# Kernel optimization log

Hardware: AMD Instinct MI355X
Metric: run time of the kernel (lower is better)

## Reference

```python
import jax, jax.numpy as jnp
import numpy as np

W_SEG = 2048   # segment_length w
R = 4          # dilation r
H = 16         # num_attention_heads


def setup_inputs() -> dict:
    key = jax.random.key(0)
    k0, k1, k2 = jax.random.split(key, 3)
    B, S, Hid = 2, 8192, 1024
    X = jax.random.normal(k0, (B, S, Hid), dtype=jnp.float32)
    Wq = jax.random.normal(k1, (Hid, Hid), dtype=jnp.float32) * 0.02
    bq = jnp.zeros((Hid,), jnp.float32)
    Wkv = jax.random.normal(k2, (Hid, 2 * Hid), dtype=jnp.float32) * 0.02
    bkv = jnp.zeros((2 * Hid,), jnp.float32)
    return {"X": X, "Wq": Wq, "bq": bq, "Wkv": Wkv, "bkv": bkv}


def reference(X, Wq, bq, Wkv, bkv):
    B, S, Hid = X.shape
    D = Hid // H                      # head dim
    num_points = W_SEG // R           # tokens kept per segment
    num_seg = S // W_SEG
    scale = 1.0 / np.sqrt(D).astype(np.float32)

    q = (X @ Wq + bq).reshape(B, S, H, D)
    kv = (X @ Wkv + bkv).reshape(B, S, 2, H, D)
    k, v = kv[:, :, 0], kv[:, :, 1]

    # dilated base indices: segment offset + r-strided points -> [num_seg*num_points]
    base = (jnp.arange(num_seg)[:, None] * W_SEG
            + jnp.arange(num_points)[None, :] * R).reshape(-1)
    shift = jnp.arange(H) % R                       # per-head shift
    idx = base[None, :] + shift[:, None]            # [H, T']
    Tq = idx.shape[1]
    idxT = idx.T                                    # [T', H]
    head_ix = jnp.arange(H)[None, :]                # [1, H] -> broadcasts with idxT

    # per-head dilated gather: sparse[b, t, h, d] = full[b, idx[h, t], h, d]
    sq = q[:, idxT, head_ix, :]                     # [B, T', H, D]
    sk = k[:, idxT, head_ix, :]
    sv = v[:, idxT, head_ix, :]

    sq = sq.reshape(B, num_seg, num_points, H, D)
    sk = sk.reshape(B, num_seg, num_points, H, D)
    sv = sv.reshape(B, num_seg, num_points, H, D)

    # per-segment (non-causal) attention, same math as flash_attn_kvpacked_func
    scores = jnp.einsum('bsqhd,bskhd->bshqk', sq, sk) * scale
    probs = jax.nn.softmax(scores, axis=-1)
    ctx = jnp.einsum('bshqk,bskhd->bsqhd', probs, sv)
    ctx = ctx.reshape(B, Tq, H, D)

    # scatter back into zeros at the gathered positions (unique per head)
    out = jnp.zeros((B, S, H, D), ctx.dtype).at[:, idxT, head_ix, :].set(ctx)
    return out.reshape(B, S, Hid)
```

## Files before the change

kernel.cpp:

```cpp
#include <hip/hip_runtime.h>

typedef unsigned short u16;
typedef unsigned int   u32;
typedef __bf16 bf16x8 __attribute__((ext_vector_type(8)));
typedef float  f32x4  __attribute__((ext_vector_type(4)));
typedef short  s16x4  __attribute__((ext_vector_type(4)));

#define QSCALE 0.125f

__device__ __forceinline__ u16 f2bf(float f) {
  union { float f; u32 u; } a; a.f = f;
  u32 u = a.u;
  u = (u + 0x7FFFu + ((u >> 16) & 1u)) >> 16;
  return (u16)u;
}

__device__ __forceinline__ void async16(const void* g, void* l) {
  __builtin_amdgcn_global_load_lds(
      (const __attribute__((address_space(1))) void*)g,
      (__attribute__((address_space(3))) void*)l, 16, 0, 0);
}

__global__ __launch_bounds__(256) void pack_w(const float* __restrict__ Wq,
                                              const float* __restrict__ Wkv,
                                              u16* __restrict__ Wp,
                                              const float* __restrict__ bq,
                                              const float* __restrict__ bkv,
                                              float* __restrict__ bp) {
  __shared__ float tile[32][65];
  int bx = blockIdx.x;
  if (bx >= 1536) {
    int idx = (bx - 1536) * 256 + threadIdx.x;
    int r = idx / 768, n = idx % 768;
    int t = n >> 8, hh = (n >> 6) & 3, d = n & 63;
    int h = hh * 4 + r;
    float v = (t == 0) ? bq[h * 64 + d] * QSCALE
            : (t == 1) ? bkv[h * 64 + d]
                       : bkv[1024 + h * 64 + d];
    bp[idx] = v;
    return;
  }
  int ks = bx & 31; int rem = bx >> 5;
  int hh = rem & 3; rem >>= 2;
  int t  = rem % 3; int r = rem / 3;
  int h  = hh * 4 + r;
  const float* src; int rs, cb;
  if (t == 0)      { src = Wq;  rs = 1024; cb = h * 64; }
  else if (t == 1) { src = Wkv; rs = 2048; cb = h * 64; }
  else             { src = Wkv; rs = 2048; cb = 1024 + h * 64; }
  int tid = threadIdx.x;
  {
    int kk = tid >> 3, dd = (tid & 7) << 3;
    const float* s0 = src + (size_t)(ks * 32 + kk) * rs + cb + dd;
    float4 a = *(const float4*)s0;
    float4 c = *(const float4*)(s0 + 4);
    tile[kk][dd + 0] = a.x; tile[kk][dd + 1] = a.y;
    tile[kk][dd + 2] = a.z; tile[kk][dd + 3] = a.w;
    tile[kk][dd + 4] = c.x; tile[kk][dd + 5] = c.y;
    tile[kk][dd + 6] = c.z; tile[kk][dd + 7] = c.w;
  }
  __syncthreads();
  {
    int d = tid >> 2, kc = tid & 3;
    float sc = (t == 0) ? QSCALE : 1.0f;
    u32 w[4];
#pragma unroll
    for (int j = 0; j < 4; ++j) {
      u16 lo = f2bf(tile[kc * 8 + 2 * j][d] * sc);
      u16 hi = f2bf(tile[kc * 8 + 2 * j + 1][d] * sc);
      w[j] = (u32)lo | ((u32)hi << 16);
    }
    int n = t * 256 + hh * 64 + d;
    int Nt = n >> 7, nt = (n >> 4) & 7, nn = n & 15;
    size_t off = (size_t)r * 786432 + (size_t)Nt * 131072 +
                 (size_t)ks * 4096 + nt * 512 + kc * 128 + nn * 8;
    uint4 o; o.x = w[0]; o.y = w[1]; o.z = w[2]; o.w = w[3];
    *(uint4*)(Wp + off) = o;
  }
}

__global__ __launch_bounds__(256, 3) void gemm1(const float* __restrict__ X,
                                                const u16* __restrict__ Wp,
                                                const float* __restrict__ bp,
                                                u16* __restrict__ Qd,
                                                u16* __restrict__ Kd,
                                                u16* __restrict__ Vd) {
  __shared__ u16 ldsAB[8192];
  u16* ldsA = ldsAB;
  u16* ldsB = ldsAB + 4096;
  int bx = blockIdx.x;
  int xcd = bx & 7;
  int idx = bx >> 3;
  int r = xcd >> 1;
  int Mtile = (xcd & 1) * 16 + (idx / 6);
  int Ntile = idx % 6;
  int tid = threadIdx.x, w = tid >> 6, lane = tid & 63;
  int wr = w >> 1, wc = w & 1;
  int l15 = lane & 15, l4 = lane >> 4;

  int rl = tid >> 1, tq = tid & 1;
  int srow = (Mtile >> 2) * 2048 + ((Mtile & 3) * 128 + rl) * 4 + r;
  const float* Xthr = X + (size_t)srow * 1024 + tq * 4;
  int abase = ((rl >> 4) * 64 + (rl & 15)) * 8 + tq * 4;

  const u16* Bsrc = Wp + (size_t)r * 786432 + (size_t)Ntile * 131072 +
                    w * 1024 + lane * 8;

  float4 ar[4];
#pragma unroll
  for (int it = 0; it < 4; ++it) ar[it] = *(const float4*)(Xthr + it * 8);

  f32x4 acc[4][4] = {};
  for (int ks = 0; ks < 32; ++ks) {
    __syncthreads();
#pragma unroll
    for (int it = 0; it < 4; ++it) {
      u32 x0 = __float_as_uint(ar[it].x) + 0x8000u;
      u32 x1 = __float_as_uint(ar[it].y) + 0x8000u;
      u32 x2 = __float_as_uint(ar[it].z) + 0x8000u;
      u32 x3 = __float_as_uint(ar[it].w) + 0x8000u;
      u32 lo = __builtin_amdgcn_perm(x1, x0, 0x07060302u);
      u32 hi = __builtin_amdgcn_perm(x3, x2, 0x07060302u);
      uint2 d2; d2.x = lo; d2.y = hi;
      *(uint2*)&ldsA[abase + it * 128] = d2;
    }
    const u16* b = Bsrc + ks * 4096;
    async16(b,       &ldsB[w * 1024]);
    async16(b + 512, &ldsB[w * 1024 + 512]);
    if (ks < 31) {
      const float* xn = Xthr + (ks + 1) * 32;
#pragma unroll
      for (int it = 0; it < 4; ++it) ar[it] = *(const float4*)(xn + it * 8);
    }
    __syncthreads();
    bf16x8 af[4], bf[4];
#pragma unroll
    for (int i = 0; i < 4; ++i)
      af[i] = *(const bf16x8*)&ldsA[((wr * 4 + i) * 64 + lane) * 8];
#pragma unroll
    for (int j = 0; j < 4; ++j)
      bf[j] = *(const bf16x8*)&ldsB[((wc * 4 + j) * 64 + lane) * 8];
#pragma unroll
    for (int i = 0; i < 4; ++i)
#pragma unroll
      for (int j = 0; j < 4; ++j)
        acc[i][j] = __builtin_amdgcn_mfma_f32_16x16x32_bf16(af[i], bf[j],
                                                            acc[i][j], 0, 0, 0);
  }

  int nb = Ntile * 128 + wc * 64;
  int t = nb >> 8, hh = (nb >> 6) & 3;
  int h = hh * 4 + r;
  u16* T = (t == 0) ? Qd : ((t == 1) ? Kd : Vd);
  float biasv[4];
#pragma unroll
  for (int j = 0; j < 4; ++j) biasv[j] = bp[r * 768 + nb + j * 16 + l15];

  u16* eb = ldsAB + w * 1152;
  int rrow = lane >> 2, seg = lane & 3;
#pragma unroll
  for (int i = 0; i < 4; ++i) {
    __syncthreads();
#pragma unroll
    for (int j = 0; j < 4; ++j)
#pragma unroll
      for (int reg = 0; reg < 4; ++reg)
        eb[(l4 * 4 + reg) * 72 + j * 16 + l15] = f2bf(acc[i][j][reg] + biasv[j]);
    __syncthreads();
    uint4 d0 = *(const uint4*)&eb[rrow * 72 + seg * 16];
    uint4 d1 = *(const uint4*)&eb[rrow * 72 + seg * 16 + 8];
    int m = Mtile * 128 + wr * 64 + i * 16 + rrow;
    int bseg = m >> 9, p = m & 511;
    size_t off = ((size_t)(bseg * 16 + h) * 512 + p) * 64 + seg * 16;
    *(uint4*)(T + off) = d0;
    *(uint4*)(T + off + 8) = d1;
  }
}

__global__ __launch_bounds__(512, 4) void attn(const u16* __restrict__ Qd,
                                               const u16* __restrict__ Kd,
                                               const u16* __restrict__ Vd,
                                               float* __restrict__ out) {
  __shared__ u16 ldsK[128 * 72];
  __shared__ u16 ldsV[64 * 136];
  int bx = blockIdx.x;
  int unit = bx & 127, qq = bx >> 7;
  int b = unit >> 6, seg = (unit >> 4) & 3, h = unit & 15;
  int tid = threadIdx.x, w = tid >> 6, lane = tid & 63;
  int l15 = lane & 15, l4 = lane >> 4;
  const u16* Qu = Qd + (size_t)unit * 32768;
  const u16* Ku = Kd + (size_t)unit * 32768;
  const u16* Vu = Vd + (size_t)unit * 32768;

  int q0 = qq * 128 + w * 16;
  bf16x8 qf[2];
#pragma unroll
  for (int hf = 0; hf < 2; ++hf)
    qf[hf] = *(const bf16x8*)(Qu + (q0 + l15) * 64 + hf * 32 + l4 * 8);

  f32x4 O[4] = {};
  float lrun = 0.f;

  int c0 = tid, c1 = 512 + tid;
  int kp0 = c0 >> 3, kd0 = c0 & 7;
  int kp1 = c1 >> 3, kd1 = c1 & 7;
  int vd0 = (c0 & 7) << 3, vd1 = (c1 & 7) << 3;

  uint4 kreg0 = *(const uint4*)(Ku + c0 * 8);
  uint4 kreg1 = *(const uint4*)(Ku + c1 * 8);
  uint4 vreg0 = *(const uint4*)(Vu + c0 * 8);
  uint4 vreg1 = *(const uint4*)(Vu + c1 * 8);

  for (int ch = 0; ch < 4; ++ch) {
    __syncthreads();
    *(uint4*)&ldsK[kp0 * 72 + kd0 * 8] = kreg0;
    *(uint4*)&ldsK[kp1 * 72 + kd1 * 8] = kreg1;
    {
      u32 ww0[4] = {vreg0.x, vreg0.y, vreg0.z, vreg0.w};
      u32 ww1[4] = {vreg1.x, vreg1.y, vreg1.z, vreg1.w};
#pragma unroll
      for (int j = 0; j < 4; ++j) {
        ldsV[(vd0 + 2 * j) * 136 + kp0]     = (u16)(ww0[j] & 0xFFFFu);
        ldsV[(vd0 + 2 * j + 1) * 136 + kp0] = (u16)(ww0[j] >> 16);
        ldsV[(vd1 + 2 * j) * 136 + kp1]     = (u16)(ww1[j] & 0xFFFFu);
        ldsV[(vd1 + 2 * j + 1) * 136 + kp1] = (u16)(ww1[j] >> 16);
      }
    }
    __syncthreads();
    if (ch < 3) {
      const u16* Ksn = Ku + (ch + 1) * 8192;
      const u16* Vsn = Vu + (ch + 1) * 8192;
      kreg0 = *(const uint4*)(Ksn + c0 * 8);
      kreg1 = *(const uint4*)(Ksn + c1 * 8);
      vreg0 = *(const uint4*)(Vsn + c0 * 8);
      vreg1 = *(const uint4*)(Vsn + c1 * 8);
    }

    float csum = 0.f;
    s16x4 pk[8];
#pragma unroll
    for (int kt = 0; kt < 8; ++kt) {
      bf16x8 a0 = *(const bf16x8*)&ldsK[(kt * 16 + l15) * 72 + l4 * 8];
      bf16x8 a1 = *(const bf16x8*)&ldsK[(kt * 16 + l15) * 72 + 32 + l4 * 8];
      f32x4 s = __builtin_amdgcn_mfma_f32_16x16x32_bf16(
          a0, qf[0], (f32x4){0.f, 0.f, 0.f, 0.f}, 0, 0, 0);
      s = __builtin_amdgcn_mfma_f32_16x16x32_bf16(a1, qf[1], s, 0, 0, 0);
      float e0 = __expf(s[0]);
      float e1 = __expf(s[1]);
      float e2 = __expf(s[2]);
      float e3 = __expf(s[3]);
      csum += (e0 + e1) + (e2 + e3);
      s16x4 pv;
      pv[0] = (short)(__float_as_uint(e0) >> 16);
      pv[1] = (short)(__float_as_uint(e1) >> 16);
      pv[2] = (short)(__float_as_uint(e2) >> 16);
      pv[3] = (short)(__float_as_uint(e3) >> 16);
      pk[kt] = pv;
    }
    csum += __shfl_xor(csum, 16, 64);
    csum += __shfl_xor(csum, 32, 64);
    lrun += csum;
#pragma unroll
    for (int kt = 0; kt < 8; ++kt)
#pragma unroll
      for (int dn = 0; dn < 4; ++dn) {
        s16x4 vb = *(const s16x4*)&ldsV[(dn * 16 + l15) * 136 + kt * 16 + l4 * 4];
        O[dn] = __builtin_amdgcn_mfma_f32_16x16x16bf16_1k(pk[kt], vb,
                                                          O[dn], 0, 0, 0);
      }
  }

  {
    float rl = __builtin_amdgcn_rcpf(lrun);
#pragma unroll
    for (int reg = 0; reg < 4; ++reg) {
      float rr = __shfl(rl, l4 * 4 + reg, 64);
      int p = q0 + l4 * 4 + reg;
      int spos = seg * 2048 + p * 4 + (h & 3);
      size_t base = ((size_t)(b * 8192 + spos)) * 1024 + h * 64 + l15;
#pragma unroll
      for (int dn = 0; dn < 4; ++dn)
        out[base + dn * 16] = O[dn][reg] * rr;
    }
  }

  {
    int row_i = bx * 32 + (tid >> 4);
    int sub = tid & 15;
    int rr = row_i & 3;
    float4 z = {0.f, 0.f, 0.f, 0.f};
    float* rowp = out + (size_t)row_i * 1024 + sub * 4;
#pragma unroll
    for (int hz = 0; hz < 16; ++hz) {
      if ((hz & 3) == rr) continue;
      *(float4*)(rowp + hz * 64) = z;
    }
  }
}

extern "C" void kernel_launch(void* const* d_in, const int* in_sizes, int n_in,
                              void* d_out, int out_size, void* d_ws, size_t ws_size,
                              hipStream_t stream) {
  (void)in_sizes; (void)n_in; (void)ws_size; (void)out_size;
  const float* X   = (const float*)d_in[0];
  const float* Wq  = (const float*)d_in[1];
  const float* bq  = (const float*)d_in[2];
  const float* Wkv = (const float*)d_in[3];
  const float* bkv = (const float*)d_in[4];
  float* out = (float*)d_out;
  char* ws = (char*)d_ws;
  u16*  Wp = (u16*)(ws);
  float* bp = (float*)(ws + 6291456);
  u16*  Qd = (u16*)(ws + 6303744);
  u16*  Kd = (u16*)(ws + 14692352);
  u16*  Vd = (u16*)(ws + 23080960);

  pack_w <<<1548, 256, 0, stream>>>(Wq, Wkv, Wp, bq, bkv, bp);
  gemm1  <<<768,  256, 0, stream>>>(X, Wp, bp, Qd, Kd, Vd);
  attn   <<<512,  512, 0, stream>>>(Qd, Kd, Vd, out);
}
```

Baseline: 187.6 us.

## Double-buffer LDS tiles in projection GEMM to overlap loads with MFMA

Splits the projection GEMM's shared-memory staging into two A and two B buffers so the next k-step's converted X tile and async weight load are written while MFMAs consume the current buffers. This removes one of the two barriers per k-step and hides load latency. The X load pattern is also changed to wider contiguous 16-float chunks per thread with 16-byte LDS stores. It doubles LDS use per block, which may affect occupancy, and relies on the barrier to order the async LDS loads.

```diff
diff --git a/kernel.cpp b/kernel.cpp
--- a/kernel.cpp
+++ b/kernel.cpp
@@ -13,6 +13,12 @@
   u32 u = a.u;
   u = (u + 0x7FFFu + ((u >> 16) & 1u)) >> 16;
   return (u16)u;
+}
+
+__device__ __forceinline__ u32 pack2bf(float a, float b) {
+  u32 xa = __float_as_uint(a) + 0x8000u;
+  u32 xb = __float_as_uint(b) + 0x8000u;
+  return __builtin_amdgcn_perm(xb, xa, 0x07060302u);
 }
 
 __device__ __forceinline__ void async16(const void* g, void* l) {
@@ -85,9 +91,11 @@
                                                 u16* __restrict__ Qd,
                                                 u16* __restrict__ Kd,
                                                 u16* __restrict__ Vd) {
-  __shared__ u16 ldsAB[8192];
-  u16* ldsA = ldsAB;
-  u16* ldsB = ldsAB + 4096;
+  __shared__ u16 lds[16384];
+  u16* bufA0 = lds;
+  u16* bufA1 = lds + 4096;
+  u16* bufB0 = lds + 8192;
+  u16* bufB1 = lds + 12288;
   int bx = blockIdx.x;
   int xcd = bx & 7;
   int idx = bx >> 3;
@@ -98,48 +106,63 @@
   int wr = w >> 1, wc = w & 1;
   int l15 = lane & 15, l4 = lane >> 4;
 
-  int rl = tid >> 1, tq = tid & 1;
+  int mt = tid >> 5, mm = (tid >> 1) & 15, khalf = tid & 1;
+  int rl = mt * 16 + mm;
   int srow = (Mtile >> 2) * 2048 + ((Mtile & 3) * 128 + rl) * 4 + r;
-  const float* Xthr = X + (size_t)srow * 1024 + tq * 4;
-  int abase = ((rl >> 4) * 64 + (rl & 15)) * 8 + tq * 4;
+  const float* Xthr = X + (size_t)srow * 1024 + khalf * 16;
+  int acell = (mt * 64 + mm) * 8 + khalf * 256;
 
   const u16* Bsrc = Wp + (size_t)r * 786432 + (size_t)Ntile * 131072 +
                     w * 1024 + lane * 8;
 
   float4 ar[4];
 #pragma unroll
-  for (int it = 0; it < 4; ++it) ar[it] = *(const float4*)(Xthr + it * 8);
+  for (int i = 0; i < 4; ++i) ar[i] = *(const float4*)(Xthr + i * 4);
+  {
+    uint4 c0, c1;
+    c0.x = pack2bf(ar[0].x, ar[0].y); c0.y = pack2bf(ar[0].z, ar[0].w);
+    c0.z = pack2bf(ar[1].x, ar[1].y); c0.w = pack2bf(ar[1].z, ar[1].w);
+    c1.x = pack2bf(ar[2].x, ar[2].y); c1.y = pack2bf(ar[2].z, ar[2].w);
+    c1.z = pack2bf(ar[3].x, ar[3].y); c1.w = pack2bf(ar[3].z, ar[3].w);
+    *(uint4*)&bufA0[acell] = c0;
+    *(uint4*)&bufA0[acell + 128] = c1;
+  }
+  async16(Bsrc,       &bufB0[w * 1024]);
+  async16(Bsrc + 512, &bufB0[w * 1024 + 512]);
+#pragma unroll
+  for (int i = 0; i < 4; ++i) ar[i] = *(const float4*)(Xthr + 32 + i * 4);
 
   f32x4 acc[4][4] = {};
   for (int ks = 0; ks < 32; ++ks) {
-    __syncthreads();
-#pragma unroll
-    for (int it = 0; it < 4; ++it) {
-      u32 x0 = __float_as_uint(ar[it].x) + 0x8000u;
-      u32 x1 = __float_as_uint(ar[it].y) + 0x8000u;
-      u32 x2 = __float_as_uint(ar[it].z) + 0x8000u;
-      u32 x3 = __float_as_uint(ar[it].w) + 0x8000u;
-      u32 lo = __builtin_amdgcn_perm(x1, x0, 0x07060302u);
-      u32 hi = __builtin_amdgcn_perm(x3, x2, 0x07060302u);
-      uint2 d2; d2.x = lo; d2.y = hi;
-      *(uint2*)&ldsA[abase + it * 128] = d2;
-    }
-    const u16* b = Bsrc + ks * 4096;
-    async16(b,       &ldsB[w * 1024]);
-    async16(b + 512, &ldsB[w * 1024 + 512]);
+    u16* bA = (ks & 1) ? bufA1 : bufA0;
+    u16* bB = (ks & 1) ? bufB1 : bufB0;
+    __syncthreads();
     if (ks < 31) {
-      const float* xn = Xthr + (ks + 1) * 32;
-#pragma unroll
-      for (int it = 0; it < 4; ++it) ar[it] = *(const float4*)(xn + it * 8);
-    }
-    __syncthreads();
+      u16* nA = (ks & 1) ? bufA0 : bufA1;
+      u16* nB = (ks & 1) ? bufB0 : bufB1;
+      uint4 c0, c1;
+      c0.x = pack2bf(ar[0].x, ar[0].y); c0.y = pack2bf(ar[0].z, ar[0].w);
+      c0.z = pack2bf(ar[1].x, ar[1].y); c0.w = pack2bf(ar[1].z, ar[1].w);
+      c1.x = pack2bf(ar[2].x, ar[2].y); c1.y = pack2bf(ar[2].z, ar[2].w);
+      c1.z = pack2bf(ar[3].x, ar[3].y); c1.w = pack2bf(ar[3].z, ar[3].w);
+      *(uint4*)&nA[acell] = c0;
+      *(uint4*)&nA[acell + 128] = c1;
+      const u16* b = Bsrc + (ks + 1) * 4096;
+      async16(b,       &nB[w * 1024]);
+      async16(b + 512, &nB[w * 1024 + 512]);
+      if (ks < 30) {
+        const float* xn = Xthr + (ks + 2) * 32;
+#pragma unroll
+        for (int i = 0; i < 4; ++i) ar[i] = *(const float4*)(xn + i * 4);
+      }
+    }
     bf16x8 af[4], bf[4];
 #pragma unroll
     for (int i = 0; i < 4; ++i)
-      af[i] = *(const bf16x8*)&ldsA[((wr * 4 + i) * 64 + lane) * 8];
+      af[i] = *(const bf16x8*)&bA[((wr * 4 + i) * 64 + lane) * 8];
 #pragma unroll
     for (int j = 0; j < 4; ++j)
-      bf[j] = *(const bf16x8*)&ldsB[((wc * 4 + j) * 64 + lane) * 8];
+      bf[j] = *(const bf16x8*)&bB[((wc * 4 + j) * 64 + lane) * 8];
 #pragma unroll
     for (int i = 0; i < 4; ++i)
 #pragma unroll
@@ -156,7 +179,7 @@
 #pragma unroll
   for (int j = 0; j < 4; ++j) biasv[j] = bp[r * 768 + nb + j * 16 + l15];
 
-  u16* eb = ldsAB + w * 1152;
+  u16* eb = lds + w * 1152;
   int rrow = lane >> 2, seg = lane & 3;
 #pragma unroll
   for (int i = 0; i < 4; ++i) {
```

Result: no change. 185.1 us (-1.3%).
